# Performance work log

Measured on AMD Instinct MI355X. Metric: run time of the kernel, lower is better.

The kernel has to match this reference:

```python
import jax, jax.numpy as jnp
import numpy as np

PAD_ID, BOS_ID, EOS_ID = 0, 2, 3
NHEAD = 8


def _sincos(T, d):
    pos = jnp.arange(T, dtype=jnp.float32)
    omega = jnp.exp(-jnp.arange(0, d, 2, dtype=jnp.float32) * (np.log(10000.0) / d))
    out = pos[:, None] * omega[None, :]  # [T, d/2]
    return jnp.stack([jnp.sin(out), jnp.cos(out)], axis=2).reshape(T, d)[None]  # [1,T,d]


def _ln(x, g, b, eps=1e-5):
    mu = x.mean(-1, keepdims=True)
    var = ((x - mu) ** 2).mean(-1, keepdims=True)
    return (x - mu) / jnp.sqrt(var + eps) * g + b


def _mha(q_in, kv_in, wqkv, bqkv, wo, bo, mask):
    B, Tq, d = q_in.shape
    Tk = kv_in.shape[1]
    hd = d // NHEAD
    q = q_in @ wqkv[:d].T + bqkv[:d]
    k = kv_in @ wqkv[d:2 * d].T + bqkv[d:2 * d]
    v = kv_in @ wqkv[2 * d:].T + bqkv[2 * d:]
    q = q.reshape(B, Tq, NHEAD, hd).transpose(0, 2, 1, 3)
    k = k.reshape(B, Tk, NHEAD, hd).transpose(0, 2, 1, 3)
    v = v.reshape(B, Tk, NHEAD, hd).transpose(0, 2, 1, 3)
    s = jnp.einsum('bhqd,bhkd->bhqk', q, k) / np.sqrt(hd)
    if mask is not None:
        s = s + mask
    a = jax.nn.softmax(s, axis=-1)
    o = jnp.einsum('bhqk,bhkd->bhqd', a, v).transpose(0, 2, 1, 3).reshape(B, Tq, d)
    return o @ wo.T + bo


def _last_logits(tokens, state, emb_table, qkv_w, qkv_b, out_w, out_b,
                 ffn_w1, ffn_b1, ffn_w2, ffn_b2, ln_g, ln_b):
    T = tokens.shape[1]
    d = emb_table.shape[1]
    x = emb_table[tokens] * np.sqrt(d) + _sincos(T, d)
    mask = jnp.where(jnp.tril(jnp.ones((T, T), bool)), 0.0, -jnp.inf)
    L = qkv_w.shape[0]
    for l in range(L):
        x = _ln(x + _mha(x, x, qkv_w[l, 0], qkv_b[l, 0], out_w[l, 0], out_b[l, 0], mask), ln_g[l, 0], ln_b[l, 0])
        x = _ln(x + _mha(x, state, qkv_w[l, 1], qkv_b[l, 1], out_w[l, 1], out_b[l, 1], None), ln_g[l, 1], ln_b[l, 1])
        h = jax.nn.gelu(x @ ffn_w1[l].T + ffn_b1[l], approximate=False)
        x = _ln(x + h @ ffn_w2[l].T + ffn_b2[l], ln_g[l, 2], ln_b[l, 2])
    return x[:, -1, :] @ emb_table.T  # tied output projection


def setup_inputs() -> dict:
    key = jax.random.key(0)
    ks = jax.random.split(key, 8)
    V, d, L, dff, B, K = 32000, 512, 4, 2048, 8, 64
    s = 0.02
    emb = jax.random.normal(ks[1], (V, d), jnp.float32) * s
    emb = emb.at[PAD_ID].set(0.0)  # padding_idx row is zero
    return {
        'state': jax.random.normal(ks[0], (B, K, d), jnp.float32),
        'emb_table': emb,
        'qkv_w': jax.random.normal(ks[2], (L, 2, 3 * d, d), jnp.float32) * s,
        'qkv_b': jnp.zeros((L, 2, 3 * d), jnp.float32),
        'out_w': jax.random.normal(ks[3], (L, 2, d, d), jnp.float32) * s,
        'out_b': jnp.zeros((L, 2, d), jnp.float32),
        'ffn_w1': jax.random.normal(ks[4], (L, dff, d), jnp.float32) * s,
        'ffn_b1': jnp.zeros((L, dff), jnp.float32),
        'ffn_w2': jax.random.normal(ks[5], (L, d, dff), jnp.float32) * s,
        'ffn_b2': jnp.zeros((L, d), jnp.float32),
        'ln_g': jnp.ones((L, 3, d), jnp.float32),
        'ln_b': jnp.zeros((L, 3, d), jnp.float32),
        'max_length': 16,
        'top_k': 50,
    }


def reference(state, emb_table, qkv_w, qkv_b, out_w, out_b, ffn_w1, ffn_b1,
              ffn_w2, ffn_b2, ln_g, ln_b, max_length, top_k):
    B = state.shape[0]
    generated = jnp.full((B, 1), BOS_ID, dtype=jnp.int32)
    finished = jnp.zeros(B, dtype=bool)
    key = jax.random.key(1)
    temperature = 1.0
    for t in range(max_length):
        # faithful naive recompute: full self+cross attention over generated prefix
        logits = _last_logits(generated, state, emb_table, qkv_w, qkv_b, out_w, out_b,
                              ffn_w1, ffn_b1, ffn_w2, ffn_b2, ln_g, ln_b)
        logits = logits / max(temperature, 1e-8)
        thr = jax.lax.top_k(logits, top_k)[0][:, -1:]
        filt = jnp.where(logits < thr, -jnp.inf, logits)
        nxt = jax.random.categorical(jax.random.fold_in(key, t), filt, axis=-1)
        nxt = jnp.where(finished, PAD_ID, nxt).astype(jnp.int32)
        generated = jnp.concatenate([generated, nxt[:, None]], axis=1)
        finished = finished | (nxt == EOS_ID)
    return generated
```

## Files before the change

kernel.cpp:

```cpp
#include <hip/hip_runtime.h>
#include <math.h>
#include <stdint.h>

#define D     512
#define DFF   2048
#define BB    8
#define NH    8
#define HD    64
#define NV    32000
#define NL    4
#define TMAX  17
#define KC    64
#define STEPS 16
#define KTOP  50
#define PAD_ID 0
#define BOS_ID 2
#define EOS_ID 3
#define SCOPE __HIP_MEMORY_SCOPE_AGENT

__device__ __forceinline__ float ld1(const float* p) {
  return __hip_atomic_load(p, __ATOMIC_RELAXED, SCOPE);
}
__device__ __forceinline__ void st1(float* p, float v) {
  __hip_atomic_store(p, v, __ATOMIC_RELAXED, SCOPE);
}
__device__ __forceinline__ float2 ld2(const float* p) {
  union { double d; float2 f; } u;
  u.d = __hip_atomic_load((const double*)p, __ATOMIC_RELAXED, SCOPE);
  return u.f;
}
__device__ __forceinline__ unsigned ldu(const unsigned* p) {
  return __hip_atomic_load(p, __ATOMIC_RELAXED, SCOPE);
}

__device__ __forceinline__ void tf2x32(unsigned k0, unsigned k1, unsigned x0, unsigned x1,
                                       unsigned& o0, unsigned& o1)
{
  unsigned ks2 = k0 ^ k1 ^ 0x1BD11BDAu;
#define TFR(r) { x0 += x1; x1 = (x1 << (r)) | (x1 >> (32 - (r))); x1 ^= x0; }
  x0 += k0; x1 += k1;
  TFR(13) TFR(15) TFR(26) TFR(6)
  x0 += k1;  x1 += ks2 + 1u;
  TFR(17) TFR(29) TFR(16) TFR(24)
  x0 += ks2; x1 += k0 + 2u;
  TFR(13) TFR(15) TFR(26) TFR(6)
  x0 += k0;  x1 += k1 + 3u;
  TFR(17) TFR(29) TFR(16) TFR(24)
  x0 += k1;  x1 += ks2 + 4u;
  TFR(13) TFR(15) TFR(26) TFR(6)
  o0 = x0 + ks2; o1 = x1 + k0 + 5u;
#undef TFR
}

__device__ __forceinline__ float wredf(float v) {
  for (int o = 32; o; o >>= 1) v += __shfl_xor(v, o, 64);
  return v;
}
__device__ __forceinline__ float wredmaxf(float v) {
  for (int o = 32; o; o >>= 1) v = fmaxf(v, __shfl_xor(v, o, 64));
  return v;
}
__device__ __forceinline__ unsigned monok(float f) {
  unsigned u = __float_as_uint(f);
  return (u & 0x80000000u) ? ~u : (u | 0x80000000u);
}

#define DOT8(a0,a1,x0,x1) (a0.x*x0.x + a0.y*x0.y + a0.z*x0.z + a0.w*x0.w + \
                           a1.x*x1.x + a1.y*x1.y + a1.z*x1.z + a1.w*x1.w)

__global__ void init_k(int* toks, unsigned* bars)
{
  int i = threadIdx.x;
  if (i < BB) toks[i * TMAX] = BOS_ID;
  for (int k = i; k < 2048; k += 256) bars[k] = 0u;
}

__global__ void cross_kv_k(const float* __restrict__ state, const float* __restrict__ qkvw,
                           const float* __restrict__ qkvb, float* __restrict__ cK,
                           float* __restrict__ cV)
{
  int gx = blockIdx.x, b = blockIdx.y, tid = threadIdx.x;
  int jblk = gx & 31, kpos = (gx >> 5) & 63, l = gx >> 11;
  int w = tid >> 6, lane = tid & 63;
  __shared__ __align__(16) float xsh[D];
  xsh[tid] = state[((size_t)b * KC + kpos) * D + tid];
  xsh[tid + 256] = state[((size_t)b * KC + kpos) * D + tid + 256];
  __syncthreads();
  for (int i = 0; i < 8; i++) {
    int j = jblk * 32 + w * 8 + i;
    int row = D + j;
    const float4* wr = (const float4*)(qkvw + (((size_t)l * 2 + 1) * (3 * D) + row) * D);
    const float4* x4 = (const float4*)xsh;
    float acc = 0.f;
    for (int e = lane; e < 128; e += 64) {
      float4 a = wr[e], xx = x4[e];
      acc += a.x * xx.x + a.y * xx.y + a.z * xx.z + a.w * xx.w;
    }
    acc = wredf(acc);
    if (lane == 0) {
      float v = acc + qkvb[((size_t)l * 2 + 1) * (3 * D) + row];
      float* dst = (j < D) ? cK : cV;
      int jj = (j < D) ? j : j - D;
      dst[(((size_t)l * BB + b) * KC + kpos) * D + jj] = v;
    }
  }
}

extern "C" __global__ void __launch_bounds__(512, 2)
decode_k(const float* __restrict__ emb, const float* __restrict__ qkv_w,
         const float* __restrict__ qkv_b, const float* __restrict__ out_w,
         const float* __restrict__ out_b, const float* __restrict__ f_w1,
         const float* __restrict__ f_b1, const float* __restrict__ f_w2,
         const float* __restrict__ f_b2, const float* __restrict__ lng,
         const float* __restrict__ lnb,
         const float* __restrict__ cK, const float* __restrict__ cV,
         float* Kc, float* Vc, float* qS, float* q2S,
         float* xt2, float* xt3, float* xt4, float* hB,
         float* xcur, float* lg, unsigned* bars, int* toks)
{
  const int tid = threadIdx.x, bid = blockIdx.x;
  const int g = bid & 7, gid = bid >> 3;
  const int w = tid >> 6, lane = tid & 63;
  unsigned gp = 0, glp = 0;
  int finished = 0;

  __shared__ __align__(16) unsigned char smem[65280];
  float* F = (float*)smem;
  float* sX1 = F;
  float* sX2 = F + 512;
  float* sQ  = F + 1024;
  float* sS  = F + 1536;
  float* sSP = F + 2080;
  float* sAO = F + 2624;
  float* sH  = F + 3136;
  float* sL  = F;
  float* sRed = F + 5184;
  unsigned short* key16 = (unsigned short*)smem;
  unsigned* histA = (unsigned*)(smem + 64000);
  unsigned* sKeys = (unsigned*)(smem + 64000);
  unsigned* sMeta = (unsigned*)(smem + 65024);
  float*    sWin  = (float*)(smem + 65056);
  int*      sWix  = (int*)(smem + 65088);

  const float SQD = (float)22.627416997969522;
  const float PEC = (float)(9.210340371976184 / 512.0);
  const float SQRT2 = (float)1.4142135623730951;

  auto gbarg = [&]() {
    asm volatile("s_waitcnt vmcnt(0)" ::: "memory");
    __syncthreads();
    ++gp;
    if (tid == 0) {
      unsigned* c = bars + g * 128;
      __hip_atomic_fetch_add(&c[(gid & 3) * 32], 1u, __ATOMIC_RELAXED, SCOPE);
      unsigned tgt = gp * 8u;
      for (;;) {
        unsigned s0 = ldu(&c[0]), s1 = ldu(&c[32]), s2 = ldu(&c[64]), s3 = ldu(&c[96]);
        unsigned mn = s0 < s1 ? s0 : s1;
        unsigned mn2 = s2 < s3 ? s2 : s3;
        if ((mn < mn2 ? mn : mn2) >= tgt) break;
        __builtin_amdgcn_s_sleep(1);
      }
    }
    asm volatile("" ::: "memory");
    __syncthreads();
  };
  auto gbarall = [&]() {
    asm volatile("s_waitcnt vmcnt(0)" ::: "memory");
    __syncthreads();
    ++glp;
    if (tid == 0) {
      unsigned* c = bars + 1024;
      __hip_atomic_fetch_add(&c[(bid & 15) * 32], 1u, __ATOMIC_RELAXED, SCOPE);
      unsigned tgt = glp * 16u;
      for (;;) {
        unsigned mn = 0xFFFFFFFFu;
#pragma unroll
        for (int i = 0; i < 16; i++) { unsigned x = ldu(&c[i * 32]); mn = x < mn ? x : mn; }
        if (mn >= tgt) break;
        __builtin_amdgcn_s_sleep(1);
      }
    }
    asm volatile("" ::: "memory");
    __syncthreads();
  };

  auto ln_local = [&](const float* src, const float* gamma, const float* beta, float* dst) {
    float v = ld1(src + tid);
    float s = wredf(v);
    if (lane == 0) sRed[w] = s;
    __syncthreads();
    float mu = (sRed[0] + sRed[1] + sRed[2] + sRed[3] +
                sRed[4] + sRed[5] + sRed[6] + sRed[7]) * (1.0f / 512.0f);
    __syncthreads();
    float d0 = v - mu;
    float q = wredf(d0 * d0);
    if (lane == 0) sRed[w] = q;
    __syncthreads();
    float sd = sqrtf((sRed[0] + sRed[1] + sRed[2] + sRed[3] +
                      sRed[4] + sRed[5] + sRed[6] + sRed[7]) * (1.0f / 512.0f) + 1e-5f);
    dst[tid] = d0 / sd * gamma[tid] + beta[tid];
    __syncthreads();
  };

  if (gid == 0) {
    float pe = (tid & 1) ? 1.0f : 0.0f;
    st1(&xcur[g * D + tid], emb[(size_t)BOS_ID * D + tid] * SQD + pe);
  }
  gbarg();

  for (int t = 0; t < STEPS; ++t) {
    const int T = t + 1;
    for (int l = 0; l < NL; ++l) {
      const float* wqkv0 = qkv_w + ((size_t)l * 2 + 0) * (3 * D) * D;
      const float* bqkv0 = qkv_b + ((size_t)l * 2 + 0) * (3 * D);
      const float* wqkv1 = qkv_w + ((size_t)l * 2 + 1) * (3 * D) * D;
      const float* bqkv1 = qkv_b + ((size_t)l * 2 + 1) * (3 * D);
      const float* wo0 = out_w + ((size_t)l * 2 + 0) * D * D;
      const float* bo0 = out_b + ((size_t)l * 2 + 0) * D;
      const float* wo1 = out_w + ((size_t)l * 2 + 1) * D * D;
      const float* bo1 = out_b + ((size_t)l * 2 + 1) * D;

      if (l == 0) {
        sX1[tid] = ld1(&xcur[g * D + tid]);
        __syncthreads();
      } else {
        ln_local(&xt4[g * D], lng + ((size_t)(l - 1) * 3 + 2) * D,
                 lnb + ((size_t)(l - 1) * 3 + 2) * D, sX1);
      }
      {
        const float4 x0 = ((const float4*)sX1)[lane], x1v = ((const float4*)sX1)[lane + 64];
        const int jbase = gid * 48 + w * 6;
        float4 wa[6], wb[6];
#pragma unroll
        for (int r = 0; r < 6; ++r) {
          const float4* w4 = (const float4*)(wqkv0 + (size_t)(jbase + r) * D);
          wa[r] = w4[lane]; wb[r] = w4[lane + 64];
        }
        float acc[6];
#pragma unroll
        for (int r = 0; r < 6; ++r) acc[r] = DOT8(wa[r], wb[r], x0, x1v);
#pragma unroll
        for (int o = 32; o; o >>= 1) {
#pragma unroll
          for (int r = 0; r < 6; ++r) acc[r] += __shfl_xor(acc[r], o, 64);
        }
        if (lane == 0) {
#pragma unroll
          for (int r = 0; r < 6; ++r) {
            int j = jbase + r;
            float v = acc[r] + bqkv0[j];
            if (j < D)          st1(&qS[g * D + j], v);
            else if (j < 2 * D) st1(&Kc[(((size_t)l * BB + g) * TMAX + t) * D + (j - D)], v);
            else                st1(&Vc[(((size_t)l * BB + g) * TMAX + t) * D + (j - 2 * D)], v);
          }
        }
      }
      gbarg();

      sQ[tid] = ld1(&qS[g * D + tid]);
      __syncthreads();
      if (tid < NH * T) {
        int h = tid / T, k = tid - h * T;
        const float4* Kr = (const float4*)(Kc + (((size_t)l * BB + g) * TMAX + k) * D + h * HD);
        const float4* q4 = (const float4*)(sQ + h * HD);
        float sc = 0.f;
#pragma unroll
        for (int e = 0; e < 16; ++e) {
          float4 a = Kr[e], b2 = q4[e];
          sc += a.x * b2.x + a.y * b2.y + a.z * b2.z + a.w * b2.w;
        }
        sS[h * TMAX + k] = sc * 0.125f;
      }
      __syncthreads();
      {
        int h = w;
        float v = (lane < T) ? sS[h * TMAX + lane] : -INFINITY;
        float m = wredmaxf(v);
        float p = (lane < T) ? expf(v - m) : 0.f;
        float den = wredf(p);
        if (lane < T) sSP[h * TMAX + lane] = p / den;
      }
      __syncthreads();
      {
        int h = w;
        const float* Vb = Vc + (((size_t)l * BB + g) * TMAX) * D + h * HD + lane;
        float acc = 0.f;
        for (int k = 0; k < T; ++k) acc += sSP[h * TMAX + k] * Vb[(size_t)k * D];
        sAO[tid] = acc;
      }
      __syncthreads();
      {
        const float4 x0 = ((const float4*)sAO)[lane], x1v = ((const float4*)sAO)[lane + 64];
        const int jbase = gid * 16 + w * 2;
        float4 wa[2], wb[2];
#pragma unroll
        for (int r = 0; r < 2; ++r) {
          const float4* w4 = (const float4*)(wo0 + (size_t)(jbase + r) * D);
          wa[r] = w4[lane]; wb[r] = w4[lane + 64];
        }
        float acc[2];
#pragma unroll
        for (int r = 0; r < 2; ++r) acc[r] = DOT8(wa[r], wb[r], x0, x1v);
#pragma unroll
        for (int o = 32; o; o >>= 1) {
#pragma unroll
          for (int r = 0; r < 2; ++r) acc[r] += __shfl_xor(acc[r], o, 64);
        }
        if (lane == 0) {
#pragma unroll
          for (int r = 0; r < 2; ++r) {
            int j = jbase + r;
            st1(&xt2[g * D + j], acc[r] + bo0[j] + sX1[j]);
          }
        }
      }
      gbarg();

      ln_local(&xt2[g * D], lng + ((size_t)l * 3 + 0) * D, lnb + ((size_t)l * 3 + 0) * D, sX2);
      {
        const float4 x0 = ((const float4*)sX2)[lane], x1v = ((const float4*)sX2)[lane + 64];
        const int jbase = gid * 16 + w * 2;
        float4 wa[2], wb[2];
#pragma unroll
        for (int r = 0; r < 2; ++r) {
          const float4* w4 = (const float4*)(wqkv1 + (size_t)(jbase + r) * D);
          wa[r] = w4[lane]; wb[r] = w4[lane + 64];
        }
        float acc[2];
#pragma unroll
        for (int r = 0; r < 2; ++r) acc[r] = DOT8(wa[r], wb[r], x0, x1v);
#pragma unroll
        for (int o = 32; o; o >>= 1) {
#pragma unroll
          for (int r = 0; r < 2; ++r) acc[r] += __shfl_xor(acc[r], o, 64);
        }
        if (lane == 0) {
#pragma unroll
          for (int r = 0; r < 2; ++r) {
            int j = jbase + r;
            st1(&q2S[g * D + j], acc[r] + bqkv1[j]);
          }
        }
      }
      gbarg();

      sQ[tid] = ld1(&q2S[g * D + tid]);
      __syncthreads();
      {
        int h = w, k = lane;
        const float4* Kr = (const float4*)(cK + (((size_t)l * BB + g) * KC + k) * D + h * HD);
        const float4* q4 = (const float4*)(sQ + h * HD);
        float sc = 0.f;
#pragma unroll
        for (int e = 0; e < 16; ++e) {
          float4 a = Kr[e], b2 = q4[e];
          sc += a.x * b2.x + a.y * b2.y + a.z * b2.z + a.w * b2.w;
        }
        sS[h * 64 + k] = sc * 0.125f;
      }
      __syncthreads();
      {
        int h = w;
        float v = sS[h * 64 + lane];
        float m = wredmaxf(v);
        float p = expf(v - m);
        float den = wredf(p);
        sSP[h * 64 + lane] = p / den;
      }
      __syncthreads();
      {
        int h = w;
        const float* Vb = cV + (((size_t)l * BB + g) * KC) * D + h * HD + lane;
        float acc = 0.f;
        for (int k = 0; k < KC; ++k) acc += sSP[h * 64 + k] * Vb[(size_t)k * D];
        sAO[tid] = acc;
      }
      __syncthreads();
      {
        const float4 x0 = ((const float4*)sAO)[lane], x1v = ((const float4*)sAO)[lane + 64];
        const int jbase = gid * 16 + w * 2;
        float4 wa[2], wb[2];
#pragma unroll
        for (int r = 0; r < 2; ++r) {
          const float4* w4 = (const float4*)(wo1 + (size_t)(jbase + r) * D);
          wa[r] = w4[lane]; wb[r] = w4[lane + 64];
        }
        float acc[2];
#pragma unroll
        for (int r = 0; r < 2; ++r) acc[r] = DOT8(wa[r], wb[r], x0, x1v);
#pragma unroll
        for (int o = 32; o; o >>= 1) {
#pragma unroll
          for (int r = 0; r < 2; ++r) acc[r] += __shfl_xor(acc[r], o, 64);
        }
        if (lane == 0) {
#pragma unroll
          for (int r = 0; r < 2; ++r) {
            int j = jbase + r;
            st1(&xt3[g * D + j], acc[r] + bo1[j] + sX2[j]);
          }
        }
      }
      gbarg();

      ln_local(&xt3[g * D], lng + ((size_t)l * 3 + 1) * D, lnb + ((size_t)l * 3 + 1) * D, sX1);
      {
        const float4 x0 = ((const float4*)sX1)[lane], x1v = ((const float4*)sX1)[lane + 64];
        const int jbase = gid * 64 + w * 8;
        float4 wa[8], wb[8];
#pragma unroll
        for (int r = 0; r < 8; ++r) {
          const float4* w4 = (const float4*)(f_w1 + (size_t)l * DFF * D + (size_t)(jbase + r) * D);
          wa[r] = w4[lane]; wb[r] = w4[lane + 64];
        }
        float acc[8];
#pragma unroll
        for (int r = 0; r < 8; ++r) acc[r] = DOT8(wa[r], wb[r], x0, x1v);
#pragma unroll
        for (int o = 32; o; o >>= 1) {
#pragma unroll
          for (int r = 0; r < 8; ++r) acc[r] += __shfl_xor(acc[r], o, 64);
        }
        if (lane == 0) {
#pragma unroll
          for (int r = 0; r < 8; ++r) {
            int j = jbase + r;
            float v = acc[r] + f_b1[(size_t)l * DFF + j];
            v = v * (erff(v / SQRT2) + 1.0f) / 2.0f;
            st1(&hB[g * DFF + j], v);
          }
        }
      }
      gbarg();

      for (int ii = tid; ii < 1024; ii += 512) {
        float2 v = ld2(&hB[g * DFF + 2 * ii]);
        sH[2 * ii] = v.x; sH[2 * ii + 1] = v.y;
      }
      __syncthreads();
      {
        float4 hx[8];
#pragma unroll
        for (int e = 0; e < 8; ++e) hx[e] = ((const float4*)sH)[lane + e * 64];
        const int jbase = gid * 16 + w * 2;
        float acc[2];
#pragma unroll
        for (int r = 0; r < 2; ++r) {
          const float4* w4 = (const float4*)(f_w2 + (size_t)l * D * DFF + (size_t)(jbase + r) * DFF);
          float a = 0.f;
#pragma unroll
          for (int e = 0; e < 8; ++e) {
            float4 aw = w4[lane + e * 64];
            a += aw.x * hx[e].x + aw.y * hx[e].y + aw.z * hx[e].z + aw.w * hx[e].w;
          }
          acc[r] = a;
        }
#pragma unroll
        for (int o = 32; o; o >>= 1) {
#pragma unroll
          for (int r = 0; r < 2; ++r) acc[r] += __shfl_xor(acc[r], o, 64);
        }
        if (lane == 0) {
#pragma unroll
          for (int r = 0; r < 2; ++r) {
            int j = jbase + r;
            st1(&xt4[g * D + j], acc[r] + f_b2[(size_t)l * D + j] + sX1[j]);
          }
        }
      }
      if (l < NL - 1) gbarg(); else gbarall();
    }

    for (int ii = tid; ii < 2048; ii += 512) {
      float2 v = ld2(&xt4[2 * ii]);
      sL[2 * ii] = v.x; sL[2 * ii + 1] = v.y;
    }
    __syncthreads();
    {
      int b = w;
      float vals[8]; float s = 0.f;
#pragma unroll
      for (int e = 0; e < 8; ++e) { vals[e] = sL[b * D + lane + e * 64]; s += vals[e]; }
      s = wredf(s);
      float mu = s * (1.0f / 512.0f);
      float q = 0.f;
#pragma unroll
      for (int e = 0; e < 8; ++e) { float d0 = vals[e] - mu; q += d0 * d0; }
      q = wredf(q);
      float sd = sqrtf(q * (1.0f / 512.0f) + 1e-5f);
      const float* ga = lng + 11 * D;
      const float* be = lnb + 11 * D;
#pragma unroll
      for (int e = 0; e < 8; ++e)
        sL[b * D + lane + e * 64] = (vals[e] - mu) / sd * ga[lane + e * 64] + be[lane + e * 64];
    }
    __syncthreads();
    for (int i = w; i < 125; i += 8) {
      int v = i * 256 + bid;
      const float4* er = (const float4*)(emb + (size_t)v * D);
      float4 e0 = er[lane], e1 = er[lane + 64];
      float acc[8];
#pragma unroll
      for (int b = 0; b < 8; b++) {
        const float4* x4 = (const float4*)(sL + b * D);
        float4 x0 = x4[lane], x1v = x4[lane + 64];
        acc[b] = DOT8(e0, e1, x0, x1v);
      }
#pragma unroll
      for (int o = 32; o; o >>= 1) {
#pragma unroll
        for (int b = 0; b < 8; b++) acc[b] += __shfl_xor(acc[b], o, 64);
      }
      if (lane == 0) {
#pragma unroll
        for (int b = 0; b < 8; b++) st1(&lg[(size_t)b * NV + v], acc[b]);
      }
    }
    gbarall();

    if (gid == 0) {
      int b = g;
      if (tid < 256) histA[tid] = 0u;
      __syncthreads();
      for (int v2 = tid; v2 < NV / 2; v2 += 512) {
        float2 f = ld2(&lg[(size_t)b * NV + 2 * v2]);
        unsigned u0 = monok(f.x), u1 = monok(f.y);
        key16[2 * v2] = (unsigned short)(u0 >> 16);
        key16[2 * v2 + 1] = (unsigned short)(u1 >> 16);
        atomicAdd(&histA[u0 >> 24], 1u);
        atomicAdd(&histA[u1 >> 24], 1u);
      }
      __syncthreads();
      if (tid == 0) {
        unsigned k = KTOP, cum = 0;
        for (int bin = 255; bin >= 0; bin--) {
          cum += histA[bin];
          if (cum >= k) { sMeta[0] = (unsigned)bin; sMeta[1] = k - (cum - histA[bin]); break; }
        }
      }
      __syncthreads();
      unsigned selHi = sMeta[0], rem1 = sMeta[1];
      if (tid < 256) histA[tid] = 0u;
      __syncthreads();
      for (int v = tid; v < NV; v += 512) {
        unsigned k16 = key16[v];
        if ((k16 >> 8) == selHi) atomicAdd(&histA[k16 & 255u], 1u);
      }
      __syncthreads();
      if (tid == 0) {
        unsigned k = rem1, cum = 0;
        for (int bin = 255; bin >= 0; bin--) {
          cum += histA[bin];
          if (cum >= k) { sMeta[2] = (selHi << 8) | (unsigned)bin; sMeta[1] = k - (cum - histA[bin]); break; }
        }
        sMeta[3] = 0u;
      }
      __syncthreads();
      unsigned P16 = sMeta[2], rem2 = sMeta[1];
      for (int v = tid; v < NV; v += 512) {
        if (key16[v] == (unsigned short)P16) {
          unsigned i = atomicAdd(&sMeta[3], 1u);
          if (i < 256) sKeys[i] = monok(ld1(&lg[(size_t)b * NV + v]));
        }
      }
      __syncthreads();
      if (tid == 0) {
        unsigned n = sMeta[3]; if (n > 256) n = 256;
        unsigned thr = 0;
        for (unsigned it = 0; it < rem2; ++it) {
          unsigned bestk = 0; int bj = 0;
          for (unsigned jx = 0; jx < n; jx++)
            if (sKeys[jx] > bestk) { bestk = sKeys[jx]; bj = (int)jx; }
          thr = bestk;
          sKeys[bj] = 0u;
        }
        sMeta[5] = (thr & 0x80000000u) ? (thr ^ 0x80000000u) : ~thr;
      }
      __syncthreads();
      float th = __uint_as_float(sMeta[5]);
      unsigned k0, k1;
      tf2x32(0u, 1u, 0u, (unsigned)t, k0, k1);
      float best = -INFINITY; int bi = NV;
      for (int v = tid; v < NV; v += 512) {
        if (key16[v] >= (unsigned short)P16) {
          float lo = ld1(&lg[(size_t)b * NV + v]);
          if (lo >= th) {
            unsigned o0, o1;
            tf2x32(k0, k1, 0u, (unsigned)(b * NV + v), o0, o1);
            unsigned bits = o0 ^ o1;
            unsigned ub = (bits >> 9) | 0x3f800000u;
            float fu = __uint_as_float(ub) - 1.0f;
            const float TINY = 1.17549435e-38f;
            float u = fu * (1.0f - TINY) + TINY;
            u = fmaxf(TINY, u);
            float gmb = -logf(-logf(u));
            float s = lo + gmb;
            if (s > best || (s == best && v < bi)) { best = s; bi = v; }
          }
        }
      }
      for (int o = 32; o; o >>= 1) {
        float ob = __shfl_xor(best, o, 64); int ox = __shfl_xor(bi, o, 64);
        if (ob > best || (ob == best && ox < bi)) { best = ob; bi = ox; }
      }
      if (lane == 0) { sWin[w] = best; sWix[w] = bi; }
      __syncthreads();
      if (tid == 0) {
        float bb = sWin[0]; int bx = sWix[0];
        for (int i2 = 1; i2 < 8; i2++) {
          if (sWin[i2] > bb || (sWin[i2] == bb && sWix[i2] < bx)) { bb = sWin[i2]; bx = sWix[i2]; }
        }
        int tok = bx;
        if (finished) tok = PAD_ID;
        toks[b * TMAX + t + 1] = tok;
        if (tok == EOS_ID) finished = 1;
        sMeta[4] = (unsigned)tok;
      }
      __syncthreads();
      {
        int tok = (int)sMeta[4];
        float omega = expf(-(float)(tid & ~1) * PEC);
        float val = (float)(t + 1) * omega;
        float pe = (tid & 1) ? cosf(val) : sinf(val);
        st1(&xcur[g * D + tid], emb[(size_t)tok * D + tid] * SQD + pe);
      }
    }
    gbarg();
  }
}

extern "C" void kernel_launch(void* const* d_in, const int* in_sizes, int n_in,
                              void* d_out, int out_size, void* d_ws, size_t ws_size,
                              hipStream_t stream)
{
  const float* state = (const float*)d_in[0];
  const float* emb   = (const float*)d_in[1];
  const float* qkv_w = (const float*)d_in[2];
  const float* qkv_b = (const float*)d_in[3];
  const float* out_w = (const float*)d_in[4];
  const float* out_b = (const float*)d_in[5];
  const float* f_w1  = (const float*)d_in[6];
  const float* f_b1  = (const float*)d_in[7];
  const float* f_w2  = (const float*)d_in[8];
  const float* f_b2  = (const float*)d_in[9];
  const float* lng   = (const float*)d_in[10];
  const float* lnb   = (const float*)d_in[11];

  float* ws = (float*)d_ws;
  float* cK   = ws;
  float* cV   = cK + (size_t)NL * BB * KC * D;
  float* Kc   = cV + (size_t)NL * BB * KC * D;
  float* Vc   = Kc + (size_t)NL * BB * TMAX * D;
  float* qS   = Vc + (size_t)NL * BB * TMAX * D;
  float* q2S  = qS + BB * D;
  float* xt2  = q2S + BB * D;
  float* xt3  = xt2 + BB * D;
  float* xt4  = xt3 + BB * D;
  float* hB   = xt4 + BB * D;
  float* xcur = hB + BB * DFF;
  float* lg   = xcur + BB * D;
  unsigned* bars = (unsigned*)(lg + (size_t)BB * NV);

  int* toks = (int*)d_out;

  init_k<<<1, 256, 0, stream>>>(toks, bars);
  cross_kv_k<<<dim3(NL * KC * 32, BB), 256, 0, stream>>>(state, qkv_w, qkv_b, cK, cV);
  decode_k<<<256, 512, 0, stream>>>(emb, qkv_w, qkv_b, out_w, out_b,
                                    f_w1, f_b1, f_w2, f_b2, lng, lnb,
                                    cK, cV, Kc, Vc, qS, q2S,
                                    xt2, xt3, xt4, hB, xcur, lg, bars, toks);
}
```

Before: 6.056 ms.

## Process two batch rows per block group to halve weight reads, doubling grid

```diff
diff --git a/kernel.cpp b/kernel.cpp
--- a/kernel.cpp
+++ b/kernel.cpp
@@ -5,6 +5,7 @@
 #define D     512
 #define DFF   2048
 #define BB    8
+#define NB    2
 #define NH    8
 #define HD    64
 #define NV    32000
@@ -106,7 +107,7 @@
   }
 }
 
-extern "C" __global__ void __launch_bounds__(512, 2)
+extern "C" __global__ void __launch_bounds__(512, 4)
 decode_k(const float* __restrict__ emb, const float* __restrict__ qkv_w,
          const float* __restrict__ qkv_b, const float* __restrict__ out_w,
          const float* __restrict__ out_b, const float* __restrict__ f_w1,
@@ -119,7 +120,12 @@
          float* xcur, float* lg, unsigned* bars, int* toks)
 {
   const int tid = threadIdx.x, bid = blockIdx.x;
-  const int g = bid & 7, gid = bid >> 3;
+  const int xcd = bid & 7;
+  const int g2 = xcd >> 1;
+  const int half = xcd & 1;
+  const int hid = bid >> 3;
+  const int gid = hid * 2 + half;
+  const int b0 = g2 * 2, b1 = b0 + 1;
   const int w = tid >> 6, lane = tid & 63;
   unsigned gp = 0, glp = 0;
   int finished = 0;
@@ -127,14 +133,14 @@
   __shared__ __align__(16) unsigned char smem[65280];
   float* F = (float*)smem;
   float* sX1 = F;
-  float* sX2 = F + 512;
-  float* sQ  = F + 1024;
-  float* sS  = F + 1536;
-  float* sSP = F + 2080;
-  float* sAO = F + 2624;
-  float* sH  = F + 3136;
+  float* sX2 = F + 1024;
+  float* sQ  = F + 2048;
+  float* sAO = F + 3072;
+  float* sS  = F + 4096;
+  float* sSP = F + 5184;
+  float* sH  = F + 6272;
+  float* sRed = F + 10368;
   float* sL  = F;
-  float* sRed = F + 5184;
   unsigned short* key16 = (unsigned short*)smem;
   unsigned* histA = (unsigned*)(smem + 64000);
   unsigned* sKeys = (unsigned*)(smem + 64000);
@@ -151,9 +157,9 @@
     __syncthreads();
     ++gp;
     if (tid == 0) {
-      unsigned* c = bars + g * 128;
+      unsigned* c = bars + g2 * 256;
       __hip_atomic_fetch_add(&c[(gid & 3) * 32], 1u, __ATOMIC_RELAXED, SCOPE);
-      unsigned tgt = gp * 8u;
+      unsigned tgt = gp * 32u;
       for (;;) {
         unsigned s0 = ldu(&c[0]), s1 = ldu(&c[32]), s2 = ldu(&c[64]), s3 = ldu(&c[96]);
         unsigned mn = s0 < s1 ? s0 : s1;
@@ -172,7 +178,7 @@
     if (tid == 0) {
       unsigned* c = bars + 1024;
       __hip_atomic_fetch_add(&c[(bid & 15) * 32], 1u, __ATOMIC_RELAXED, SCOPE);
-      unsigned tgt = glp * 16u;
+      unsigned tgt = glp * 32u;
       for (;;) {
         unsigned mn = 0xFFFFFFFFu;
 #pragma unroll
@@ -185,27 +191,28 @@
     __syncthreads();
   };
 
-  auto ln_local = [&](const float* src, const float* gamma, const float* beta, float* dst) {
-    float v = ld1(src + tid);
-    float s = wredf(v);
+  auto ln2 = [&](const float* srcbase, const float* gamma, const float* beta, float* dst) {
+    int nb = tid >> 8, e = tid & 255;
+    const float* sp = srcbase + (size_t)(b0 + nb) * D;
+    float v0 = ld1(sp + e), v1 = ld1(sp + e + 256);
+    float s = wredf(v0 + v1);
     if (lane == 0) sRed[w] = s;
     __syncthreads();
-    float mu = (sRed[0] + sRed[1] + sRed[2] + sRed[3] +
-                sRed[4] + sRed[5] + sRed[6] + sRed[7]) * (1.0f / 512.0f);
-    __syncthreads();
-    float d0 = v - mu;
-    float q = wredf(d0 * d0);
+    float mu = (sRed[nb*4] + sRed[nb*4+1] + sRed[nb*4+2] + sRed[nb*4+3]) * (1.0f/512.0f);
+    __syncthreads();
+    float d0 = v0 - mu, d1 = v1 - mu;
+    float q = wredf(d0*d0 + d1*d1);
     if (lane == 0) sRed[w] = q;
     __syncthreads();
-    float sd = sqrtf((sRed[0] + sRed[1] + sRed[2] + sRed[3] +
-                      sRed[4] + sRed[5] + sRed[6] + sRed[7]) * (1.0f / 512.0f) + 1e-5f);
-    dst[tid] = d0 / sd * gamma[tid] + beta[tid];
+    float sd = sqrtf((sRed[nb*4] + sRed[nb*4+1] + sRed[nb*4+2] + sRed[nb*4+3]) * (1.0f/512.0f) + 1e-5f);
+    dst[nb*512 + e]       = d0 / sd * gamma[e]       + beta[e];
+    dst[nb*512 + e + 256] = d1 / sd * gamma[e + 256] + beta[e + 256];
     __syncthreads();
   };
 
-  if (gid == 0) {
+  if (bid < BB) {
     float pe = (tid & 1) ? 1.0f : 0.0f;
-    st1(&xcur[g * D + tid], emb[(size_t)BOS_ID * D + tid] * SQD + pe);
+    st1(&xcur[bid * D + tid], emb[(size_t)BOS_ID * D + tid] * SQD + pe);
   }
   gbarg();
 
@@ -222,251 +229,261 @@
       const float* bo1 = out_b + ((size_t)l * 2 + 1) * D;
 
       if (l == 0) {
-        sX1[tid] = ld1(&xcur[g * D + tid]);
+        int nb = tid >> 8, e = tid & 255;
+        sX1[nb*512 + e]       = ld1(&xcur[(b0 + nb) * D + e]);
+        sX1[nb*512 + e + 256] = ld1(&xcur[(b0 + nb) * D + e + 256]);
         __syncthreads();
       } else {
-        ln_local(&xt4[g * D], lng + ((size_t)(l - 1) * 3 + 2) * D,
-                 lnb + ((size_t)(l - 1) * 3 + 2) * D, sX1);
+        ln2(xt4, lng + ((size_t)(l - 1) * 3 + 2) * D, lnb + ((size_t)(l - 1) * 3 + 2) * D, sX1);
       }
       {
-        const float4 x0 = ((const float4*)sX1)[lane], x1v = ((const float4*)sX1)[lane + 64];
-        const int jbase = gid * 48 + w * 6;
-        float4 wa[6], wb[6];
-#pragma unroll
-        for (int r = 0; r < 6; ++r) {
-          const float4* w4 = (const float4*)(wqkv0 + (size_t)(jbase + r) * D);
+        const float4* xA = (const float4*)sX1;
+        const float4* xB = (const float4*)(sX1 + 512);
+        float4 xa0 = xA[lane], xa1 = xA[lane + 64];
+        float4 xb0 = xB[lane], xb1 = xB[lane + 64];
+        int rows[3]; int nr = 0;
+        if (w < 4) rows[nr++] = gid * 4 + w;
+        rows[nr++] = 512 + hid * 16 + w * 2;
+        rows[nr++] = 513 + hid * 16 + w * 2;
+        float4 wa[3], wb[3];
+        for (int r = 0; r < nr; ++r) {
+          const float4* w4 = (const float4*)(wqkv0 + (size_t)rows[r] * D);
           wa[r] = w4[lane]; wb[r] = w4[lane + 64];
         }
-        float acc[6];
-#pragma unroll
-        for (int r = 0; r < 6; ++r) acc[r] = DOT8(wa[r], wb[r], x0, x1v);
-#pragma unroll
-        for (int o = 32; o; o >>= 1) {
-#pragma unroll
-          for (int r = 0; r < 6; ++r) acc[r] += __shfl_xor(acc[r], o, 64);
-        }
+        float aA[3], aB[3];
+        for (int r = 0; r < nr; ++r) {
+          aA[r] = DOT8(wa[r], wb[r], xa0, xa1);
+          aB[r] = DOT8(wa[r], wb[r], xb0, xb1);
+        }
+        for (int o = 32; o; o >>= 1)
+          for (int r = 0; r < nr; ++r) {
+            aA[r] += __shfl_xor(aA[r], o, 64);
+            aB[r] += __shfl_xor(aB[r], o, 64);
+          }
         if (lane == 0) {
-#pragma unroll
-          for (int r = 0; r < 6; ++r) {
-            int j = jbase + r;
-            float v = acc[r] + bqkv0[j];
-            if (j < D)          st1(&qS[g * D + j], v);
-            else if (j < 2 * D) st1(&Kc[(((size_t)l * BB + g) * TMAX + t) * D + (j - D)], v);
-            else                st1(&Vc[(((size_t)l * BB + g) * TMAX + t) * D + (j - 2 * D)], v);
+          for (int r = 0; r < nr; ++r) {
+            int j = rows[r];
+            float bv = bqkv0[j];
+            if (j < 512) {
+              st1(&qS[(size_t)b0 * D + j], aA[r] + bv);
+              st1(&qS[(size_t)b1 * D + j], aB[r] + bv);
+            } else if (j < 1024) {
+              int col = j - 512;
+              st1(&Kc[((((size_t)xcd * NL + l) * NB + 0) * TMAX + t) * D + col], aA[r] + bv);
+              st1(&Kc[((((size_t)xcd * NL + l) * NB + 1) * TMAX + t) * D + col], aB[r] + bv);
+            } else {
+              int col = j - 1024;
+              st1(&Vc[((((size_t)xcd * NL + l) * NB + 0) * TMAX + t) * D + col], aA[r] + bv);
+              st1(&Vc[((((size_t)xcd * NL + l) * NB + 1) * TMAX + t) * D + col], aB[r] + bv);
+            }
           }
         }
       }
       gbarg();
 
-      sQ[tid] = ld1(&qS[g * D + tid]);
-      __syncthreads();
-      if (tid < NH * T) {
-        int h = tid / T, k = tid - h * T;
-        const float4* Kr = (const float4*)(Kc + (((size_t)l * BB + g) * TMAX + k) * D + h * HD);
-        const float4* q4 = (const float4*)(sQ + h * HD);
+      {
+        int nb = tid >> 8, e = tid & 255;
+        sQ[nb*512 + e]       = ld1(&qS[(b0 + nb) * D + e]);
+        sQ[nb*512 + e + 256] = ld1(&qS[(b0 + nb) * D + e + 256]);
+      }
+      __syncthreads();
+      {
+        int nb = tid >> 8, tt = tid & 255;
+        if (tt < NH * T) {
+          int h = tt / T, k = tt - h * T;
+          const float4* Kr = (const float4*)(Kc + ((((size_t)xcd * NL + l) * NB + nb) * TMAX + k) * D + h * HD);
+          const float4* q4 = (const float4*)(sQ + nb*512 + h * HD);
+          float sc = 0.f;
+#pragma unroll
+          for (int e = 0; e < 16; ++e) {
+            float4 a = Kr[e], b2 = q4[e];
+            sc += a.x * b2.x + a.y * b2.y + a.z * b2.z + a.w * b2.w;
+          }
+          sS[nb*544 + h * TMAX + k] = sc * 0.125f;
+        }
+      }
+      __syncthreads();
+      {
+        int rr = w * 2 + (lane >> 5);
+        int nb = rr >> 3, h = rr & 7, l5 = lane & 31;
+        float v = (l5 < T) ? sS[nb*544 + h * TMAX + l5] : -INFINITY;
+        float m = v;
+        for (int o = 16; o; o >>= 1) m = fmaxf(m, __shfl_xor(m, o, 64));
+        float p = (l5 < T) ? expf(v - m) : 0.f;
+        float den = p;
+        for (int o = 16; o; o >>= 1) den += __shfl_xor(den, o, 64);
+        if (l5 < T) sSP[nb*544 + h * TMAX + l5] = p / den;
+      }
+      __syncthreads();
+#pragma unroll
+      for (int hf = 0; hf < 2; ++hf) {
+        int o = tid + hf * 512;
+        int nb = o >> 9, dd = o & 511, h = dd >> 6, d3 = dd & 63;
+        const float* Vb = Vc + ((((size_t)xcd * NL + l) * NB + nb) * TMAX) * D + h * HD + d3;
+        float acc = 0.f;
+        for (int k = 0; k < T; ++k) acc += sSP[nb*544 + h * TMAX + k] * Vb[(size_t)k * D];
+        sAO[nb*512 + dd] = acc;
+      }
+      __syncthreads();
+      if (w < 4) {
+        int j = gid * 4 + w;
+        const float4* w4 = (const float4*)(wo0 + (size_t)j * D);
+        float4 a0 = w4[lane], a1 = w4[lane + 64];
+        const float4* yA = (const float4*)sAO;
+        const float4* yB = (const float4*)(sAO + 512);
+        float aA = DOT8(a0, a1, yA[lane], yA[lane + 64]);
+        float aB = DOT8(a0, a1, yB[lane], yB[lane + 64]);
+        for (int o = 32; o; o >>= 1) { aA += __shfl_xor(aA, o, 64); aB += __shfl_xor(aB, o, 64); }
+        if (lane == 0) {
+          st1(&xt2[(size_t)b0 * D + j], aA + bo0[j] + sX1[j]);
+          st1(&xt2[(size_t)b1 * D + j], aB + bo0[j] + sX1[512 + j]);
+        }
+      }
+      gbarg();
+
+      ln2(xt2, lng + ((size_t)l * 3 + 0) * D, lnb + ((size_t)l * 3 + 0) * D, sX2);
+      if (w < 4) {
+        int j = gid * 4 + w;
+        const float4* w4 = (const float4*)(wqkv1 + (size_t)j * D);
+        float4 a0 = w4[lane], a1 = w4[lane + 64];
+        const float4* yA = (const float4*)sX2;
+        const float4* yB = (const float4*)(sX2 + 512);
+        float aA = DOT8(a0, a1, yA[lane], yA[lane + 64]);
+        float aB = DOT8(a0, a1, yB[lane], yB[lane + 64]);
+        for (int o = 32; o; o >>= 1) { aA += __shfl_xor(aA, o, 64); aB += __shfl_xor(aB, o, 64); }
+        if (lane == 0) {
+          st1(&q2S[(size_t)b0 * D + j], aA + bqkv1[j]);
+          st1(&q2S[(size_t)b1 * D + j], aB + bqkv1[j]);
+        }
+      }
+      gbarg();
+
+      {
+        int nb = tid >> 8, e = tid & 255;
+        sQ[nb*512 + e]       = ld1(&q2S[(b0 + nb) * D + e]);
+        sQ[nb*512 + e + 256] = ld1(&q2S[(b0 + nb) * D + e + 256]);
+      }
+      __syncthreads();
+#pragma unroll
+      for (int hf = 0; hf < 2; ++hf) {
+        int o = tid + hf * 512;
+        int nb = o >> 9, dd = o & 511, h = dd >> 6, k = dd & 63;
+        const float4* Kr = (const float4*)(cK + (((size_t)l * BB + b0 + nb) * KC + k) * D + h * HD);
+        const float4* q4 = (const float4*)(sQ + nb*512 + h * HD);
         float sc = 0.f;
 #pragma unroll
         for (int e = 0; e < 16; ++e) {
           float4 a = Kr[e], b2 = q4[e];
           sc += a.x * b2.x + a.y * b2.y + a.z * b2.z + a.w * b2.w;
         }
-        sS[h * TMAX + k] = sc * 0.125f;
-      }
-      __syncthreads();
-      {
-        int h = w;
-        float v = (lane < T) ? sS[h * TMAX + lane] : -INFINITY;
-        float m = wredmaxf(v);
-        float p = (lane < T) ? expf(v - m) : 0.f;
-        float den = wredf(p);
-        if (lane < T) sSP[h * TMAX + lane] = p / den;
-      }
-      __syncthreads();
-      {
-        int h = w;
-        const float* Vb = Vc + (((size_t)l * BB + g) * TMAX) * D + h * HD + lane;
-        float acc = 0.f;
-        for (int k = 0; k < T; ++k) acc += sSP[h * TMAX + k] * Vb[(size_t)k * D];
-        sAO[tid] = acc;
-      }
-      __syncthreads();
-      {
-        const float4 x0 = ((const float4*)sAO)[lane], x1v = ((const float4*)sAO)[lane + 64];
-        const int jbase = gid * 16 + w * 2;
-        float4 wa[2], wb[2];
-#pragma unroll
-        for (int r = 0; r < 2; ++r) {
-          const float4* w4 = (const float4*)(wo0 + (size_t)(jbase + r) * D);
-          wa[r] = w4[lane]; wb[r] = w4[lane + 64];
-        }
-        float acc[2];
-#pragma unroll
-        for (int r = 0; r < 2; ++r) acc[r] = DOT8(wa[r], wb[r], x0, x1v);
-#pragma unroll
-        for (int o = 32; o; o >>= 1) {
-#pragma unroll
-          for (int r = 0; r < 2; ++r) acc[r] += __shfl_xor(acc[r], o, 64);
-        }
-        if (lane == 0) {
-#pragma unroll
-          for (int r = 0; r < 2; ++r) {
-            int j = jbase + r;
-            st1(&xt2[g * D + j], acc[r] + bo0[j] + sX1[j]);
-          }
-        }
-      }
-      gbarg();
-
-      ln_local(&xt2[g * D], lng + ((size_t)l * 3 + 0) * D, lnb + ((size_t)l * 3 + 0) * D, sX2);
-      {
-        const float4 x0 = ((const float4*)sX2)[lane], x1v = ((const float4*)sX2)[lane + 64];
-        const int jbase = gid * 16 + w * 2;
-        float4 wa[2], wb[2];
-#pragma unroll
-        for (int r = 0; r < 2; ++r) {
-          const float4* w4 = (const float4*)(wqkv1 + (size_t)(jbase + r) * D);
-          wa[r] = w4[lane]; wb[r] = w4[lane + 64];
-        }
-        float acc[2];
-#pragma unroll
-        for (int r = 0; r < 2; ++r) acc[r] = DOT8(wa[r], wb[r], x0, x1v);
-#pragma unroll
-        for (int o = 32; o; o >>= 1) {
-#pragma unroll
-          for (int r = 0; r < 2; ++r) acc[r] += __shfl_xor(acc[r], o, 64);
-        }
-        if (lane == 0) {
-#pragma unroll
-          for (int r = 0; r < 2; ++r) {
-            int j = jbase + r;
-            st1(&q2S[g * D + j], acc[r] + bqkv1[j]);
-          }
-        }
-      }
-      gbarg();
-
-      sQ[tid] = ld1(&q2S[g * D + tid]);
-      __syncthreads();
-      {
-        int h = w, k = lane;
-        const float4* Kr = (const float4*)(cK + (((size_t)l * BB + g) * KC + k) * D + h * HD);
-        const float4* q4 = (const float4*)(sQ + h * HD);
-        float sc = 0.f;
-#pragma unroll
-        for (int e = 0; e < 16; ++e) {
-          float4 a = Kr[e], b2 = q4[e];
-          sc += a.x * b2.x + a.y * b2.y + a.z * b2.z + a.w * b2.w;
-        }
-        sS[h * 64 + k] = sc * 0.125f;
-      }
-      __syncthreads();
-      {
-        int h = w;
-        float v = sS[h * 64 + lane];
+        sS[nb*512 + h * 64 + k] = sc * 0.125f;
+      }
+      __syncthreads();
+#pragma unroll
+      for (int rr2 = 0; rr2 < 2; ++rr2) {
+        int rr = w + rr2 * 8;
+        int nb = rr >> 3, h = rr & 7;
+        float v = sS[nb*512 + h * 64 + lane];
         float m = wredmaxf(v);
         float p = expf(v - m);
         float den = wredf(p);
-        sSP[h * 64 + lane] = p / den;
-      }
-      __syncthreads();
+        sSP[nb*512 + h * 64 + lane] = p / den;
+      }
+      __syncthreads();
+#pragma unroll
+      for (int hf = 0; hf < 2; ++hf) {
+        int o = tid + hf * 512;
+        int nb = o >> 9, dd = o & 511, h = dd >> 6, d3 = dd & 63;
+        const float* Vb = cV + (((size_t)l * BB + b0 + nb) * KC) * D + h * HD + d3;
+        float acc = 0.f;
+        for (int k = 0; k < KC; ++k) acc += sSP[nb*512 + h * 64 + k] * Vb[(size_t)k * D];
+        sAO[nb*512 + dd] = acc;
+      }
+      __syncthreads();
+      if (w < 4) {
+        int j = gid * 4 + w;
+        const float4* w4 = (const float4*)(wo1 + (size_t)j * D);
+        float4 a0 = w4[lane], a1 = w4[lane + 64];
+        const float4* yA = (const float4*)sAO;
+        const float4* yB = (const float4*)(sAO + 512);
+        float aA = DOT8(a0, a1, yA[lane], yA[lane + 64]);
+        float aB = DOT8(a0, a1, yB[lane], yB[lane + 64]);
+        for (int o = 32; o; o >>= 1) { aA += __shfl_xor(aA, o, 64); aB += __shfl_xor(aB, o, 64); }
+        if (lane == 0) {
+          st1(&xt3[(size_t)b0 * D + j], aA + bo1[j] + sX2[j]);
+          st1(&xt3[(size_t)b1 * D + j], aB + bo1[j] + sX2[512 + j]);
+        }
+      }
+      gbarg();
+
+      ln2(xt3, lng + ((size_t)l * 3 + 1) * D, lnb + ((size_t)l * 3 + 1) * D, sX1);
       {
-        int h = w;
-        const float* Vb = cV + (((size_t)l * BB + g) * KC) * D + h * HD + lane;
-        float acc = 0.f;
-        for (int k = 0; k < KC; ++k) acc += sSP[h * 64 + k] * Vb[(size_t)k * D];
-        sAO[tid] = acc;
-      }
-      __syncthreads();
-      {
-        const float4 x0 = ((const float4*)sAO)[lane], x1v = ((const float4*)sAO)[lane + 64];
-        const int jbase = gid * 16 + w * 2;
+        const float4* xA = (const float4*)sX1;
+        const float4* xB = (const float4*)(sX1 + 512);
+        float4 xa0 = xA[lane], xa1 = xA[lane + 64];
+        float4 xb0 = xB[lane], xb1 = xB[lane + 64];
+        int jb = gid * 16 + w * 2;
         float4 wa[2], wb[2];
 #pragma unroll
         for (int r = 0; r < 2; ++r) {
-          const float4* w4 = (const float4*)(wo1 + (size_t)(jbase + r) * D);
+          const float4* w4 = (const float4*)(f_w1 + (size_t)l * DFF * D + (size_t)(jb + r) * D);
           wa[r] = w4[lane]; wb[r] = w4[lane + 64];
         }
-        float acc[2];
-#pragma unroll
-        for (int r = 0; r < 2; ++r) acc[r] = DOT8(wa[r], wb[r], x0, x1v);
+        float aA[2], aB[2];
+#pragma unroll
+        for (int r = 0; r < 2; ++r) {
+          aA[r] = DOT8(wa[r], wb[r], xa0, xa1);
+          aB[r] = DOT8(wa[r], wb[r], xb0, xb1);
+        }
 #pragma unroll
         for (int o = 32; o; o >>= 1) {
 #pragma unroll
-          for (int r = 0; r < 2; ++r) acc[r] += __shfl_xor(acc[r], o, 64);
+          for (int r = 0; r < 2; ++r) {
+            aA[r] += __shfl_xor(aA[r], o, 64);
+            aB[r] += __shfl_xor(aB[r], o, 64);
+          }
         }
         if (lane == 0) {
 #pragma unroll
           for (int r = 0; r < 2; ++r) {
-            int j = jbase + r;
-            st1(&xt3[g * D + j], acc[r] + bo1[j] + sX2[j]);
+            int j = jb + r;
+            float bv = f_b1[(size_t)l * DFF + j];
+            float vA = aA[r] + bv, vB = aB[r] + bv;
+            vA = vA * (erff(vA / SQRT2) + 1.0f) / 2.0f;
+            vB = vB * (erff(vB / SQRT2) + 1.0f) / 2.0f;
+            st1(&hB[(size_t)b0 * DFF + j], vA);
+            st1(&hB[(size_t)b1 * DFF + j], vB);
           }
         }
       }
       gbarg();
 
-      ln_local(&xt3[g * D], lng + ((size_t)l * 3 + 1) * D, lnb + ((size_t)l * 3 + 1) * D, sX1);
-      {
-        const float4 x0 = ((const float4*)sX1)[lane], x1v = ((const float4*)sX1)[lane + 64];
-        const int jbase = gid * 64 + w * 8;
-        float4 wa[8], wb[8];
-#pragma unroll
-        for (int r = 0; r < 8; ++r) {
-          const float4* w4 = (const float4*)(f_w1 + (size_t)l * DFF * D + (size_t)(jbase + r) * D);
-          wa[r] = w4[lane]; wb[r] = w4[lane + 64];
-        }
-        float acc[8];
-#pragma unroll
-        for (int r = 0; r < 8; ++r) acc[r] = DOT8(wa[r], wb[r], x0, x1v);
-#pragma unroll
-        for (int o = 32; o; o >>= 1) {
-#pragma unroll
-          for (int r = 0; r < 8; ++r) acc[r] += __shfl_xor(acc[r], o, 64);
-        }
+      for (int ii = tid; ii < 2048; ii += 512) {
+        int nbb = ii >> 10, ee = (ii & 1023) * 2;
+        float2 v = ld2(&hB[(size_t)(b0 + nbb) * DFF + ee]);
+        sH[nbb * 2048 + ee] = v.x; sH[nbb * 2048 + ee + 1] = v.y;
+      }
+      __syncthreads();
+      if (w < 4) {
+        int j = gid * 4 + w;
+        const float4* w4 = (const float4*)(f_w2 + (size_t)l * D * DFF + (size_t)j * DFF);
+        float4 wr[8];
+#pragma unroll
+        for (int e = 0; e < 8; ++e) wr[e] = w4[lane + e * 64];
+        const float4* hA = (const float4*)sH;
+        const float4* hBs = (const float4*)(sH + 2048);
+        float aA = 0.f, aB = 0.f;
+#pragma unroll
+        for (int e = 0; e < 8; ++e) {
+          float4 ha = hA[lane + e * 64], hb = hBs[lane + e * 64];
+          aA += wr[e].x * ha.x + wr[e].y * ha.y + wr[e].z * ha.z + wr[e].w * ha.w;
+          aB += wr[e].x * hb.x + wr[e].y * hb.y + wr[e].z * hb.z + wr[e].w * hb.w;
+        }
+        for (int o = 32; o; o >>= 1) { aA += __shfl_xor(aA, o, 64); aB += __shfl_xor(aB, o, 64); }
         if (lane == 0) {
-#pragma unroll
-          for (int r = 0; r < 8; ++r) {
-            int j = jbase + r;
-            float v = acc[r] + f_b1[(size_t)l * DFF + j];
-            v = v * (erff(v / SQRT2) + 1.0f) / 2.0f;
-            st1(&hB[g * DFF + j], v);
-          }
-        }
-      }
-      gbarg();
-
-      for (int ii = tid; ii < 1024; ii += 512) {
-        float2 v = ld2(&hB[g * DFF + 2 * ii]);
-        sH[2 * ii] = v.x; sH[2 * ii + 1] = v.y;
-      }
-      __syncthreads();
-      {
-        float4 hx[8];
-#pragma unroll
-        for (int e = 0; e < 8; ++e) hx[e] = ((const float4*)sH)[lane + e * 64];
-        const int jbase = gid * 16 + w * 2;
-        float acc[2];
-#pragma unroll
-        for (int r = 0; r < 2; ++r) {
-          const float4* w4 = (const float4*)(f_w2 + (size_t)l * D * DFF + (size_t)(jbase + r) * DFF);
-          float a = 0.f;
-#pragma unroll
-          for (int e = 0; e < 8; ++e) {
-            float4 aw = w4[lane + e * 64];
-            a += aw.x * hx[e].x + aw.y * hx[e].y + aw.z * hx[e].z + aw.w * hx[e].w;
-          }
-          acc[r] = a;
-        }
-#pragma unroll
-        for (int o = 32; o; o >>= 1) {
-#pragma unroll
-          for (int r = 0; r < 2; ++r) acc[r] += __shfl_xor(acc[r], o, 64);
-        }
-        if (lane == 0) {
-#pragma unroll
-          for (int r = 0; r < 2; ++r) {
-            int j = jbase + r;
-            st1(&xt4[g * D + j], acc[r] + f_b2[(size_t)l * D + j] + sX1[j]);
-          }
+          float bv = f_b2[(size_t)l * D + j];
+          st1(&xt4[(size_t)b0 * D + j], aA + bv + sX1[j]);
+          st1(&xt4[(size_t)b1 * D + j], aB + bv + sX1[512 + j]);
         }
       }
       if (l < NL - 1) gbarg(); else gbarall();
@@ -496,31 +513,33 @@
         sL[b * D + lane + e * 64] = (vals[e] - mu) / sd * ga[lane + e * 64] + be[lane + e * 64];
     }
     __syncthreads();
-    for (int i = w; i < 125; i += 8) {
-      int v = i * 256 + bid;
-      const float4* er = (const float4*)(emb + (size_t)v * D);
-      float4 e0 = er[lane], e1 = er[lane + 64];
-      float acc[8];
-#pragma unroll
-      for (int b = 0; b < 8; b++) {
-        const float4* x4 = (const float4*)(sL + b * D);
-        float4 x0 = x4[lane], x1v = x4[lane + 64];
-        acc[b] = DOT8(e0, e1, x0, x1v);
-      }
-#pragma unroll
-      for (int o = 32; o; o >>= 1) {
-#pragma unroll
-        for (int b = 0; b < 8; b++) acc[b] += __shfl_xor(acc[b], o, 64);
-      }
-      if (lane == 0) {
-#pragma unroll
-        for (int b = 0; b < 8; b++) st1(&lg[(size_t)b * NV + v], acc[b]);
+    for (int i = w; i < 63; i += 8) {
+      int v = i * 512 + bid;
+      if (v < NV) {
+        const float4* er = (const float4*)(emb + (size_t)v * D);
+        float4 e0 = er[lane], e1 = er[lane + 64];
+        float acc[8];
+#pragma unroll
+        for (int b = 0; b < 8; b++) {
+          const float4* x4 = (const float4*)(sL + b * D);
+          float4 x0 = x4[lane], x1v = x4[lane + 64];
+          acc[b] = DOT8(e0, e1, x0, x1v);
+        }
+#pragma unroll
+        for (int o = 32; o; o >>= 1) {
+#pragma unroll
+          for (int b = 0; b < 8; b++) acc[b] += __shfl_xor(acc[b], o, 64);
+        }
+        if (lane == 0) {
+#pragma unroll
+          for (int b = 0; b < 8; b++) st1(&lg[(size_t)b * NV + v], acc[b]);
+        }
       }
     }
     gbarall();
 
-    if (gid == 0) {
-      int b = g;
+    if (bid < BB) {
+      int b = bid;
       if (tid < 256) histA[tid] = 0u;
       __syncthreads();
       for (int v2 = tid; v2 < NV / 2; v2 += 512) {
@@ -623,7 +642,7 @@
         float omega = expf(-(float)(tid & ~1) * PEC);
         float val = (float)(t + 1) * omega;
         float pe = (tid & 1) ? cosf(val) : sinf(val);
-        st1(&xcur[g * D + tid], emb[(size_t)tok * D + tid] * SQD + pe);
+        st1(&xcur[b * D + tid], emb[(size_t)tok * D + tid] * SQD + pe);
       }
     }
     gbarg();
@@ -651,8 +670,8 @@
   float* cK   = ws;
   float* cV   = cK + (size_t)NL * BB * KC * D;
   float* Kc   = cV + (size_t)NL * BB * KC * D;
-  float* Vc   = Kc + (size_t)NL * BB * TMAX * D;
-  float* qS   = Vc + (size_t)NL * BB * TMAX * D;
+  float* Vc   = Kc + (size_t)8 * NL * NB * TMAX * D;
+  float* qS   = Vc + (size_t)8 * NL * NB * TMAX * D;
   float* q2S  = qS + BB * D;
   float* xt2  = q2S + BB * D;
   float* xt3  = xt2 + BB * D;
@@ -666,7 +685,7 @@
 
   init_k<<<1, 256, 0, stream>>>(toks, bars);
   cross_kv_k<<<dim3(NL * KC * 32, BB), 256, 0, stream>>>(state, qkv_w, qkv_b, cK, cV);
-  decode_k<<<256, 512, 0, stream>>>(emb, qkv_w, qkv_b, out_w, out_b,
+  decode_k<<<512, 512, 0, stream>>>(emb, qkv_w, qkv_b, out_w, out_b,
                                     f_w1, f_b1, f_w2, f_b2, lng, lnb,
                                     cK, cV, Kc, Vc, qS, q2S,
                                     xt2, xt3, xt4, hB, xcur, lg, bars, toks);
```

Result: slower. 9.218 ms (+52.2%).
